# Kernel tuning notes

Hardware: AMD Instinct MI355X
Metric: run time of the kernel (lower is better)

The kernel has to match this reference:

```python
import jax, jax.numpy as jnp
import numpy as np

NUM_USERS = 100000
NUM_ITEMS = 50000
DIM = 128
NUM_EDGES = 600000


def setup_inputs() -> dict:
    key = jax.random.key(0)
    k1, k2, k3, k4, k5, k6 = jax.random.split(key, 6)
    u_emb = jax.random.normal(k1, (NUM_USERS, DIM), dtype=jnp.float32)
    i_emb = jax.random.normal(k2, (NUM_ITEMS, DIM), dtype=jnp.float32)
    user_idx = jax.random.randint(k3, (NUM_EDGES,), 0, NUM_USERS, dtype=jnp.int32)
    item_idx = jax.random.randint(k4, (NUM_EDGES,), 0, NUM_ITEMS, dtype=jnp.int32)
    edge_index = jnp.stack([user_idx, item_idx], axis=0)
    # weights in [0.2, 1.0] per docstring (unused in eval-mode forward)
    weights = 0.2 + 0.8 * jax.random.uniform(k5, (NUM_EDGES,), dtype=jnp.float32)
    attn_w = jax.random.normal(k6, (2 * DIM,), dtype=jnp.float32) * (1.0 / np.sqrt(2 * DIM))
    return {"u_emb": u_emb, "i_emb": i_emb, "edge_index": edge_index,
            "weights": weights, "attn_w": attn_w}


def _scatter_softmax(scores, idx, num_nodes):
    # numerically stable segment softmax over edges grouped by idx
    smax = jax.ops.segment_max(scores, idx, num_segments=num_nodes)  # [N]
    exp_s = jnp.exp(scores - smax[idx])                              # [E]
    ssum = jax.ops.segment_sum(exp_s, idx, num_segments=num_nodes)   # [N]
    return exp_s / (ssum[idx] + 1e-10)


def reference(u_emb, i_emb, edge_index, weights, attn_w):
    num_users = u_emb.shape[0]
    num_items = i_emb.shape[0]
    dim = u_emb.shape[1]
    user_idx, item_idx = edge_index[0], edge_index[1]

    # attn_projector(cat([u, i])) == u @ w_u + i @ w_i (no bias)
    w_u, w_i = attn_w[:dim], attn_w[dim:]
    raw = u_emb[user_idx] @ w_u + i_emb[item_idx] @ w_i  # [E]
    raw = jnp.where(raw >= 0, raw, 0.2 * raw)            # LeakyReLU(0.2)

    u_attn = _scatter_softmax(raw, user_idx, num_users)  # [E]
    i_attn = _scatter_softmax(raw, item_idx, num_items)  # [E]

    new_u = u_emb.at[user_idx].add(i_emb[item_idx] * u_attn[:, None])
    new_i = i_emb.at[item_idx].add(u_emb[user_idx] * i_attn[:, None])
    return new_u, new_i
```

## Files before the change

kernel.cpp:

```cpp
#include <hip/hip_runtime.h>

#define DIM 128
#define SCAN_BLK 1024

__device__ __forceinline__ unsigned short bf16rn(float f) {
    unsigned u = __float_as_uint(f);
    u += 0x7fffu + ((u >> 16) & 1u);
    return (unsigned short)(u >> 16);
}

__global__ void k_prep(const float* __restrict__ u_emb, const float* __restrict__ i_emb,
                       const float* __restrict__ attn_w, float* __restrict__ sdot,
                       ushort2* __restrict__ bemb, unsigned* __restrict__ cnt,
                       int nu, int n, int do_bf16) {
    int tid = blockIdx.x * blockDim.x + threadIdx.x;
    if (tid < n) cnt[tid] = 0u;
    int gw = tid >> 6;
    int lane = threadIdx.x & 63;
    if (gw >= n) return;
    const bool isU = gw < nu;
    const float2* row = (const float2*)(isU ? u_emb + (size_t)gw * DIM
                                            : i_emb + (size_t)(gw - nu) * DIM);
    const float2* wv  = (const float2*)(isU ? attn_w : attn_w + DIM);
    float2 a = row[lane];
    float2 b = wv[lane];
    float v = a.x * b.x + a.y * b.y;
    #pragma unroll
    for (int off = 32; off; off >>= 1) v += __shfl_down(v, off);
    if (lane == 0) sdot[gw] = v;
    if (do_bf16) {
        ushort2 h;
        h.x = bf16rn(a.x);
        h.y = bf16rn(a.y);
        bemb[(size_t)gw * (DIM / 2) + lane] = h;
    }
}

__global__ void k_count(const int* __restrict__ uidx, const int* __restrict__ iidx,
                        unsigned* __restrict__ cnt, unsigned* __restrict__ ranks,
                        int nu, int ne) {
    int e = blockIdx.x * blockDim.x + threadIdx.x;
    if (e >= ne) return;
    unsigned r0 = atomicAdd(&cnt[uidx[e]], 1u);
    unsigned r1 = atomicAdd(&cnt[nu + iidx[e]], 1u);
    ranks[e] = (r0 << 16) | (r1 & 0xffffu);
}

__global__ void k_scan1(const unsigned* __restrict__ cnt, unsigned* __restrict__ incl,
                        unsigned* __restrict__ bsum, int n) {
    __shared__ unsigned part[SCAN_BLK];
    int t = threadIdx.x;
    int j = blockIdx.x * SCAN_BLK + t;
    unsigned v = (j < n) ? cnt[j] : 0u;
    part[t] = v;
    __syncthreads();
    for (int d = 1; d < SCAN_BLK; d <<= 1) {
        unsigned w = (t >= d) ? part[t - d] : 0u;
        __syncthreads();
        part[t] += w;
        __syncthreads();
    }
    if (j < n) incl[j] = part[t];
    if (t == SCAN_BLK - 1) bsum[blockIdx.x] = part[t];
}

__global__ void k_scan2(unsigned* __restrict__ bsum, int nb) {
    __shared__ unsigned part[SCAN_BLK];
    int t = threadIdx.x;
    unsigned v = (t < nb) ? bsum[t] : 0u;
    part[t] = v;
    __syncthreads();
    for (int d = 1; d < SCAN_BLK; d <<= 1) {
        unsigned w = (t >= d) ? part[t - d] : 0u;
        __syncthreads();
        part[t] += w;
        __syncthreads();
    }
    if (t < nb) bsum[t] = part[t] - v;
}

__global__ void k_scan3(const unsigned* __restrict__ cnt, const unsigned* __restrict__ incl,
                        const unsigned* __restrict__ bsum,
                        unsigned* __restrict__ off, int n) {
    int j = blockIdx.x * blockDim.x + threadIdx.x;
    if (j >= n) return;
    off[j] = incl[j] - cnt[j] + bsum[j / SCAN_BLK];
}

__global__ void k_fill(const int* __restrict__ uidx, const int* __restrict__ iidx,
                       const unsigned* __restrict__ off, const unsigned* __restrict__ ranks,
                       int* __restrict__ nbr, int nu, int ne) {
    int e = blockIdx.x * blockDim.x + threadIdx.x;
    if (e >= ne) return;
    int u = uidx[e], i = iidx[e];
    unsigned rk = ranks[e];
    nbr[off[u]      + (rk >> 16)]     = nu + i;
    nbr[off[nu + i] + (rk & 0xffffu)] = u;
}

__global__ void k_accum_bf16(const float* __restrict__ u_emb, const float* __restrict__ i_emb,
                             const uint4* __restrict__ bemb, const float* __restrict__ sdot,
                             const unsigned* __restrict__ off, const unsigned* __restrict__ cnt,
                             const int* __restrict__ nbr,
                             float* __restrict__ out, int nu, int n) {
    int wid  = (blockIdx.x * blockDim.x + threadIdx.x) >> 6;
    int lane = threadIdx.x & 63;
    int nwav = (gridDim.x * blockDim.x) >> 6;
    int q = lane >> 4, l16 = lane & 15;

    for (int node = wid; node < n; node += nwav) {
        unsigned s = off[node];
        unsigned d = cnt[node];
        float ss = sdot[node];

        float acc[8] = {0.f, 0.f, 0.f, 0.f, 0.f, 0.f, 0.f, 0.f};
        float wsum = 0.f;

        #pragma unroll 2
        for (unsigned j = (unsigned)q; j < d; j += 4) {
            int o = nbr[s + j];
            uint4 h = bemb[(size_t)o * (DIM / 8) + l16];
            float r = ss + sdot[o];
            r = fmaxf(r, 0.2f * r);
            float w = __expf(r);
            wsum += w;
            acc[0] += w * __uint_as_float(h.x << 16);
            acc[1] += w * __uint_as_float(h.x & 0xffff0000u);
            acc[2] += w * __uint_as_float(h.y << 16);
            acc[3] += w * __uint_as_float(h.y & 0xffff0000u);
            acc[4] += w * __uint_as_float(h.z << 16);
            acc[5] += w * __uint_as_float(h.z & 0xffff0000u);
            acc[6] += w * __uint_as_float(h.w << 16);
            acc[7] += w * __uint_as_float(h.w & 0xffff0000u);
        }

        #pragma unroll
        for (int m = 16; m <= 32; m <<= 1) {
            wsum += __shfl_xor(wsum, m);
            #pragma unroll
            for (int k = 0; k < 8; ++k) acc[k] += __shfl_xor(acc[k], m);
        }

        if (q == 0) {
            float inv = 1.f / (wsum + 1e-10f);
            const float* self = (node < nu) ? u_emb + (size_t)node * DIM
                                            : i_emb + (size_t)(node - nu) * DIM;
            const float4* sr = (const float4*)self;
            float4 s0 = sr[2 * l16];
            float4 s1 = sr[2 * l16 + 1];
            s0.x += acc[0] * inv; s0.y += acc[1] * inv;
            s0.z += acc[2] * inv; s0.w += acc[3] * inv;
            s1.x += acc[4] * inv; s1.y += acc[5] * inv;
            s1.z += acc[6] * inv; s1.w += acc[7] * inv;
            float4* orow = (float4*)(out + (size_t)node * DIM);
            orow[2 * l16]     = s0;
            orow[2 * l16 + 1] = s1;
        }
    }
}

__global__ void k_accum_f32(const float* __restrict__ u_emb, const float* __restrict__ i_emb,
                            const float* __restrict__ sdot,
                            const unsigned* __restrict__ off, const unsigned* __restrict__ cnt,
                            const int* __restrict__ nbr,
                            float* __restrict__ out, int nu, int n) {
    int gw = (blockIdx.x * blockDim.x + threadIdx.x) >> 6;
    int lane = threadIdx.x & 63;
    if (gw >= n) return;
    float sd_self = sdot[gw];
    unsigned s = off[gw];
    unsigned d = cnt[gw];
    float2 acc = make_float2(0.f, 0.f);
    float wsum = 0.f;
    for (unsigned base = 0; base < d; base += 64) {
        unsigned chunk = d - base; if (chunk > 64) chunk = 64;
        int   o = 0;
        float w = 0.f;
        if (lane < (int)chunk) {
            o = nbr[s + base + lane];
            float r = sd_self + sdot[o];
            r = fmaxf(r, 0.2f * r);
            w = __expf(r);
        }
        for (unsigned j = 0; j < chunk; ++j) {
            int   oj = __shfl(o, (int)j);
            float wj = __shfl(w, (int)j);
            const float* base_ = (oj < nu) ? u_emb + (size_t)oj * DIM
                                           : i_emb + (size_t)(oj - nu) * DIM;
            float2 vj = ((const float2*)base_)[lane];
            wsum += wj;
            acc.x += wj * vj.x;
            acc.y += wj * vj.y;
        }
    }
    float inv = 1.f / (wsum + 1e-10f);
    const float* self = (gw < nu) ? u_emb + (size_t)gw * DIM
                                  : i_emb + (size_t)(gw - nu) * DIM;
    float2 sv = ((const float2*)self)[lane];
    sv.x += acc.x * inv;
    sv.y += acc.y * inv;
    ((float2*)(out + (size_t)gw * DIM))[lane] = sv;
}

extern "C" void kernel_launch(void* const* d_in, const int* in_sizes, int n_in,
                              void* d_out, int out_size, void* d_ws, size_t ws_size,
                              hipStream_t stream) {
    const float* u_emb  = (const float*)d_in[0];
    const float* i_emb  = (const float*)d_in[1];
    const int*   edge   = (const int*)d_in[2];
    const float* attn_w = (const float*)d_in[4];

    const int nu = in_sizes[0] / DIM;
    const int ni = in_sizes[1] / DIM;
    const int ne = in_sizes[3];
    const int n  = nu + ni;

    const int* uidx = edge;
    const int* iidx = edge + ne;

    float* out = (float*)d_out;

    char* ws = (char*)d_ws;
    size_t used = 0;
    auto take = [&](size_t bytes) {
        char* p = ws + used;
        used += (bytes + 15) & ~size_t(15);
        return p;
    };
    float*    sdot  = (float*)   take((size_t)n * sizeof(float));
    unsigned* cnt   = (unsigned*)take((size_t)n * sizeof(unsigned));
    unsigned* off   = (unsigned*)take((size_t)n * sizeof(unsigned));
    unsigned* incl  = (unsigned*)take((size_t)n * sizeof(unsigned));
    unsigned* bsum  = (unsigned*)take((size_t)SCAN_BLK * sizeof(unsigned));
    unsigned* ranks = (unsigned*)take((size_t)ne * sizeof(unsigned));
    int*      nbr   = (int*)     take((size_t)2 * ne * sizeof(int));
    size_t bembBytes = (size_t)n * DIM * 2;
    const int do_bf16 = (used + bembBytes <= ws_size) ? 1 : 0;
    void* bemb = do_bf16 ? (void*)take(bembBytes) : nullptr;

    const int nb = (n + SCAN_BLK - 1) / SCAN_BLK;

    k_prep<<<(n + 3) / 4, 256, 0, stream>>>(u_emb, i_emb, attn_w, sdot,
                                            (ushort2*)bemb, cnt, nu, n, do_bf16);

    k_count<<<(ne + 255) / 256, 256, 0, stream>>>(uidx, iidx, cnt, ranks, nu, ne);

    k_scan1<<<nb, SCAN_BLK, 0, stream>>>(cnt, incl, bsum, n);
    k_scan2<<<1, SCAN_BLK, 0, stream>>>(bsum, nb);
    k_scan3<<<(n + 255) / 256, 256, 0, stream>>>(cnt, incl, bsum, off, n);

    k_fill<<<(ne + 255) / 256, 256, 0, stream>>>(uidx, iidx, off, ranks, nbr, nu, ne);

    if (do_bf16)
        k_accum_bf16<<<2048, 256, 0, stream>>>(u_emb, i_emb, (const uint4*)bemb,
                                               sdot, off, cnt, nbr, out, nu, n);
    else
        k_accum_f32<<<(n + 3) / 4, 256, 0, stream>>>(u_emb, i_emb, sdot, off, cnt,
                                                     nbr, out, nu, n);
}
```

Baseline: 173.6 us.

## Fuse edge counting with row prep and read self rows from bf16 copy

Merges the edge-degree counting kernel and the per-row dot/bf16-conversion kernel into one launch split by block index, zeroing counters with a memset beforehand. The final accumulation now reads the node's own embedding from the bf16 copy instead of the fp32 input, halving those bytes. The intent is to cut launch overhead and memory traffic. The exchange is that the self term is rounded to bf16, which lowers output precision.

Result: slower. 181.5 us (+4.6%).

```diff
diff --git a/kernel.cpp b/kernel.cpp
--- a/kernel.cpp
+++ b/kernel.cpp
@@ -2,6 +2,8 @@
 
 #define DIM 128
 #define SCAN_BLK 1024
+
+typedef float f32x2 __attribute__((ext_vector_type(2)));
 
 __device__ __forceinline__ unsigned short bf16rn(float f) {
     unsigned u = __float_as_uint(f);
@@ -9,10 +11,40 @@
     return (unsigned short)(u >> 16);
 }
 
+__global__ void k_count_prep(const int* __restrict__ uidx, const int* __restrict__ iidx,
+                             unsigned* __restrict__ cnt, unsigned* __restrict__ ranks,
+                             const float* __restrict__ u_emb, const float* __restrict__ i_emb,
+                             const float* __restrict__ attn_w, float* __restrict__ sdot,
+                             unsigned* __restrict__ bemb,
+                             int nu, int n, int ne, int nbCount) {
+    if ((int)blockIdx.x < nbCount) {
+        int e = blockIdx.x * blockDim.x + threadIdx.x;
+        if (e >= ne) return;
+        unsigned r0 = atomicAdd(&cnt[uidx[e]], 1u);
+        unsigned r1 = atomicAdd(&cnt[nu + iidx[e]], 1u);
+        ranks[e] = (r0 << 16) | (r1 & 0xffffu);
+        return;
+    }
+    int gw = ((blockIdx.x - nbCount) * blockDim.x + threadIdx.x) >> 6;
+    int lane = threadIdx.x & 63;
+    if (gw >= n) return;
+    const bool isU = gw < nu;
+    const f32x2* row = (const f32x2*)(isU ? u_emb + (size_t)gw * DIM
+                                          : i_emb + (size_t)(gw - nu) * DIM);
+    const float2* wv = (const float2*)(isU ? attn_w : attn_w + DIM);
+    f32x2 a = __builtin_nontemporal_load(&row[lane]);
+    float2 b = wv[lane];
+    float v = a.x * b.x + a.y * b.y;
+    #pragma unroll
+    for (int off = 32; off; off >>= 1) v += __shfl_down(v, off);
+    if (lane == 0) sdot[gw] = v;
+    unsigned packed = (unsigned)bf16rn(a.x) | ((unsigned)bf16rn(a.y) << 16);
+    bemb[(size_t)gw * (DIM / 2) + lane] = packed;
+}
+
 __global__ void k_prep(const float* __restrict__ u_emb, const float* __restrict__ i_emb,
                        const float* __restrict__ attn_w, float* __restrict__ sdot,
-                       ushort2* __restrict__ bemb, unsigned* __restrict__ cnt,
-                       int nu, int n, int do_bf16) {
+                       unsigned* __restrict__ cnt, int nu, int n) {
     int tid = blockIdx.x * blockDim.x + threadIdx.x;
     if (tid < n) cnt[tid] = 0u;
     int gw = tid >> 6;
@@ -28,12 +60,6 @@
     #pragma unroll
     for (int off = 32; off; off >>= 1) v += __shfl_down(v, off);
     if (lane == 0) sdot[gw] = v;
-    if (do_bf16) {
-        ushort2 h;
-        h.x = bf16rn(a.x);
-        h.y = bf16rn(a.y);
-        bemb[(size_t)gw * (DIM / 2) + lane] = h;
-    }
 }
 
 __global__ void k_count(const int* __restrict__ uidx, const int* __restrict__ iidx,
@@ -98,8 +124,7 @@
     nbr[off[nu + i] + (rk & 0xffffu)] = u;
 }
 
-__global__ void k_accum_bf16(const float* __restrict__ u_emb, const float* __restrict__ i_emb,
-                             const uint4* __restrict__ bemb, const float* __restrict__ sdot,
+__global__ void k_accum_bf16(const uint4* __restrict__ bemb, const float* __restrict__ sdot,
                              const unsigned* __restrict__ off, const unsigned* __restrict__ cnt,
                              const int* __restrict__ nbr,
                              float* __restrict__ out, int nu, int n) {
@@ -143,15 +168,16 @@
 
         if (q == 0) {
             float inv = 1.f / (wsum + 1e-10f);
-            const float* self = (node < nu) ? u_emb + (size_t)node * DIM
-                                            : i_emb + (size_t)(node - nu) * DIM;
-            const float4* sr = (const float4*)self;
-            float4 s0 = sr[2 * l16];
-            float4 s1 = sr[2 * l16 + 1];
-            s0.x += acc[0] * inv; s0.y += acc[1] * inv;
-            s0.z += acc[2] * inv; s0.w += acc[3] * inv;
-            s1.x += acc[4] * inv; s1.y += acc[5] * inv;
-            s1.z += acc[6] * inv; s1.w += acc[7] * inv;
+            uint4 hs = bemb[(size_t)node * (DIM / 8) + l16];
+            float4 s0, s1;
+            s0.x = __uint_as_float(hs.x << 16)         + acc[0] * inv;
+            s0.y = __uint_as_float(hs.x & 0xffff0000u) + acc[1] * inv;
+            s0.z = __uint_as_float(hs.y << 16)         + acc[2] * inv;
+            s0.w = __uint_as_float(hs.y & 0xffff0000u) + acc[3] * inv;
+            s1.x = __uint_as_float(hs.z << 16)         + acc[4] * inv;
+            s1.y = __uint_as_float(hs.z & 0xffff0000u) + acc[5] * inv;
+            s1.z = __uint_as_float(hs.w << 16)         + acc[6] * inv;
+            s1.w = __uint_as_float(hs.w & 0xffff0000u) + acc[7] * inv;
             float4* orow = (float4*)(out + (size_t)node * DIM);
             orow[2 * l16]     = s0;
             orow[2 * l16 + 1] = s1;
@@ -238,23 +264,34 @@
     const int do_bf16 = (used + bembBytes <= ws_size) ? 1 : 0;
     void* bemb = do_bf16 ? (void*)take(bembBytes) : nullptr;
 
-    const int nb = (n + SCAN_BLK - 1) / SCAN_BLK;
-
-    k_prep<<<(n + 3) / 4, 256, 0, stream>>>(u_emb, i_emb, attn_w, sdot,
-                                            (ushort2*)bemb, cnt, nu, n, do_bf16);
-
-    k_count<<<(ne + 255) / 256, 256, 0, stream>>>(uidx, iidx, cnt, ranks, nu, ne);
-
-    k_scan1<<<nb, SCAN_BLK, 0, stream>>>(cnt, incl, bsum, n);
-    k_scan2<<<1, SCAN_BLK, 0, stream>>>(bsum, nb);
-    k_scan3<<<(n + 255) / 256, 256, 0, stream>>>(cnt, incl, bsum, off, n);
-
-    k_fill<<<(ne + 255) / 256, 256, 0, stream>>>(uidx, iidx, off, ranks, nbr, nu, ne);
-
-    if (do_bf16)
-        k_accum_bf16<<<2048, 256, 0, stream>>>(u_emb, i_emb, (const uint4*)bemb,
-                                               sdot, off, cnt, nbr, out, nu, n);
-    else
-        k_accum_f32<<<(n + 3) / 4, 256, 0, stream>>>(u_emb, i_emb, sdot, off, cnt,
-                                                     nbr, out, nu, n);
-}
+    const int nb      = (n + SCAN_BLK - 1) / SCAN_BLK;
+    const int nbCount = (ne + 255) / 256;
+    const int nbPrep  = (n + 3) / 4;
+
+    if (do_bf16) {
+        hipMemsetAsync(cnt, 0, (size_t)n * sizeof(unsigned), stream);
+
+        k_count_prep<<<nbCount + nbPrep, 256, 0, stream>>>(uidx, iidx, cnt, ranks,
+                                                           u_emb, i_emb, attn_w, sdot,
+                                                           (unsigned*)bemb,
+                                                           nu, n, ne, nbCount);
+
+        k_scan1<<<nb, SCAN_BLK, 0, stream>>>(cnt, incl, bsum, n);
+        k_scan2<<<1, SCAN_BLK, 0, stream>>>(bsum, nb);
+        k_scan3<<<(n + 255) / 256, 256, 0, stream>>>(cnt, incl, bsum, off, n);
+
+        k_fill<<<nbCount, 256, 0, stream>>>(uidx, iidx, off, ranks, nbr, nu, ne);
+
+        k_accum_bf16<<<2048, 256, 0, stream>>>((const uint4*)bemb, sdot, off, cnt,
+                                               nbr, out, nu, n);
+    } else {
+        k_prep<<<nbPrep, 256, 0, stream>>>(u_emb, i_emb, attn_w, sdot, cnt, nu, n);
+        k_count<<<nbCount, 256, 0, stream>>>(uidx, iidx, cnt, ranks, nu, ne);
+        k_scan1<<<nb, SCAN_BLK, 0, stream>>>(cnt, incl, bsum, n);
+        k_scan2<<<1, SCAN_BLK, 0, stream>>>(bsum, nb);
+        k_scan3<<<(n + 255) / 256, 256, 0, stream>>>(cnt, incl, bsum, off, n);
+        k_fill<<<nbCount, 256, 0, stream>>>(uidx, iidx, off, ranks, nbr, nu, ne);
+        k_accum_f32<<<nbPrep, 256, 0, stream>>>(u_emb, i_emb, sdot, off, cnt,
+                                                nbr, out, nu, n);
+    }
+}
```
